# Kernel tuning notes

Measured on AMD Instinct MI355X. Metric: run time of the kernel, lower is better.

## Reference

```python
import jax, jax.numpy as jnp
import numpy as np


def _gru_scan(xg, w_hh, b_hh, h0):
    """Scan a GRU (PyTorch gate order r,z,n) over time. xg: (T,B,3H) precomputed input projections."""
    def step(h, g):
        gh = h @ w_hh.T + b_hh
        i_r, i_z, i_n = jnp.split(g, 3, axis=-1)
        h_r, h_z, h_n = jnp.split(gh, 3, axis=-1)
        r = jax.nn.sigmoid(i_r + h_r)
        z = jax.nn.sigmoid(i_z + h_z)
        n = jnp.tanh(i_n + r * h_n)
        h_new = (1.0 - z) * n + z * h
        return h_new, h_new
    _, ys = jax.lax.scan(step, h0, xg)
    return ys  # (T, B, H)


def setup_inputs() -> dict:
    key = jax.random.key(0)
    ks = jax.random.split(key, 13)
    B, M, T = 64, 80, 2000
    C, H, K = 256, 256, 5
    s = 0.1
    return {
        "x": jax.random.normal(ks[0], (B, M, T), jnp.float32),
        "conv_w": jax.random.normal(ks[1], (C, M, K), jnp.float32) * s,
        "conv_b": jax.random.normal(ks[2], (C,), jnp.float32) * s,
        "w_ih_f": jax.random.normal(ks[3], (3 * H, C), jnp.float32) * s,
        "w_hh_f": jax.random.normal(ks[4], (3 * H, H), jnp.float32) * s,
        "b_ih_f": jax.random.normal(ks[5], (3 * H,), jnp.float32) * s,
        "b_hh_f": jax.random.normal(ks[6], (3 * H,), jnp.float32) * s,
        "w_ih_r": jax.random.normal(ks[7], (3 * H, C), jnp.float32) * s,
        "w_hh_r": jax.random.normal(ks[8], (3 * H, H), jnp.float32) * s,
        "b_ih_r": jax.random.normal(ks[9], (3 * H,), jnp.float32) * s,
        "b_hh_r": jax.random.normal(ks[10], (3 * H,), jnp.float32) * s,
        "clf_w": jax.random.normal(ks[11], (2, 2 * H), jnp.float32) * s,
        "clf_b": jax.random.normal(ks[12], (2,), jnp.float32) * s,
        "window_size": 100,
    }


def reference(x, conv_w, conv_b, w_ih_f, w_hh_f, b_ih_f, b_hh_f,
              w_ih_r, w_hh_r, b_ih_r, b_hh_r, clf_w, clf_b, window_size):
    # Streaming (inference_mode) branch of KWSNet, expressed incrementally:
    # per-step sliding-window conv == full valid conv; the 'bidirectional' GRU
    # with seq_len=1 per step and carried hidden == two independent GRUs both
    # scanned forward in time (one with the _reverse weight set).
    B = x.shape[0]
    K = conv_w.shape[-1]
    H = w_hh_f.shape[-1]
    # Conv1d valid + ReLU: (B, C, Tc), Tc = T - K + 1
    y = jax.lax.conv_general_dilated(x, conv_w, (1,), 'VALID',
                                     dimension_numbers=('NCH', 'OIH', 'NCH'))
    y = jax.nn.relu(y + conv_b[None, :, None])
    seq = jnp.transpose(y, (2, 0, 1))  # (Tc, B, C)
    h0 = jnp.zeros((B, H), seq.dtype)
    xg_f = seq @ w_ih_f.T + b_ih_f  # (Tc, B, 3H)
    xg_r = seq @ w_ih_r.T + b_ih_r
    enc = jnp.concatenate([
        _gru_scan(xg_f, w_hh_f, b_hh_f, h0),
        _gru_scan(xg_r, w_hh_r, b_hh_r, h0),
    ], axis=-1)  # (Tc, B, 2H)
    # Sliding mean over the last W encoder outputs (W = window_size - K + 1)
    W = window_size - K + 1
    cs = jnp.concatenate([jnp.zeros_like(enc[:1]), jnp.cumsum(enc, axis=0)], axis=0)
    means = (cs[W:] - cs[:-W]) / W  # (Tout, B, 2H), Tout = T - window_size + 1
    out = means @ clf_w.T + clf_b  # (Tout, B, 2)
    # torch stacks per-step (1, B, 2) outputs -> (Tout, 1, B, 2)
    return out[:, None, :, :]
```

## Files before the change

kernel.cpp:

```cpp
#include <hip/hip_runtime.h>
#include <hip/hip_bf16.h>


#define TT    2000
#define TC    1996
#define NB    64
#define MCH   80
#define NH    256
#define NN    1536
#define TOUT  1901
#define TCH   250
#define NCHK  8
#define CROWS (TCH * NB)

typedef _Float16 h2_t __attribute__((ext_vector_type(2)));
typedef _Float16 h8_t __attribute__((ext_vector_type(8)));
typedef float    f4_t __attribute__((ext_vector_type(4)));

#define WQSCALE 254.0f
#define INV8    (1.0f / (254.0f * 127.0f))

#define OFF_SEQC ((size_t)0)
#define OFF_XG   ((size_t)8192000)
#define OFF_WT   ((size_t)57344000)
#define OFF_WCAT ((size_t)57753600)
#define OFF_PSUM ((size_t)58540032)
#define OFF_HST  ((size_t)59561984)
#define OFF_WQ   ((size_t)59693056)
#define OFF_ENC  ((size_t)60086272)

__global__ void prep_kernel(const float* __restrict__ conv_w,
                            const float* __restrict__ wihf,
                            const float* __restrict__ wihr,
                            const float* __restrict__ whhf,
                            const float* __restrict__ whhr,
                            float* __restrict__ wT,
                            _Float16* __restrict__ wcat,
                            unsigned* __restrict__ wq) {
    int idx = blockIdx.x * 256 + threadIdx.x;
    if (idx < 400 * 256) {
        int c = idx & 255, mk = idx >> 8;
        wT[idx] = conv_w[c * 400 + mk];
    }
    int i2 = idx - 400 * 256;
    if (i2 >= 0 && i2 < NN * 256) {
        int k = i2 & 255, n = i2 >> 8;
        float v = (n < 768) ? wihf[n * 256 + k] : wihr[(n - 768) * 256 + k];
        wcat[i2] = (_Float16)v;
    }
    int i4 = idx - (400 * 256 + NN * 256);
    if (i4 >= 0 && i4 < 2 * 3 * 256 * 64) {
        int r  = i4 & 255;
        int j  = (i4 >> 8) & 63;
        int dg = i4 >> 14;
        const float* whh = (dg >= 3) ? whhr : whhf;
        int g = (dg >= 3) ? dg - 3 : dg;
        const float* wp = whh + (size_t)(g * 256 + r) * 256 + 4 * j;
        unsigned v = 0;
#pragma unroll
        for (int kk = 0; kk < 4; ++kk) {
            float q = rintf(wp[kk] * WQSCALE);
            q = fminf(fmaxf(q, -127.f), 127.f);
            v |= ((unsigned)((int)q & 0xFF)) << (8 * kk);
        }
        wq[((size_t)dg * 256 + r) * 64 + j] = v;
    }
}

__global__ __launch_bounds__(256, 2)
void conv_kernel(const float* __restrict__ x, const float* __restrict__ wT,
                 const float* __restrict__ conv_b, _Float16* __restrict__ seqc,
                 int t_base, int t_len) {
    __shared__ float xs[MCH][68];
    int tile = blockIdx.x;
    int b    = blockIdx.y;
    int tid  = threadIdx.x;
    for (int idx = tid; idx < MCH * 68; idx += 256) {
        int m = idx / 68, i = idx - m * 68;
        int tt = t_base + tile * 64 + i;
        xs[m][i] = (tt < TT) ? x[(size_t)b * (MCH * TT) + m * TT + tt] : 0.f;
    }
    __syncthreads();
    int lane = tid & 63, tg = tid >> 6;
    float acc[4][16];
#pragma unroll
    for (int cq = 0; cq < 4; ++cq)
#pragma unroll
        for (int t = 0; t < 16; ++t) acc[cq][t] = 0.f;

    for (int m = 0; m < MCH; ++m) {
        float xr_[20];
#pragma unroll
        for (int q = 0; q < 5; ++q) {
            float4 v = *(const float4*)&xs[m][tg * 16 + q * 4];
            xr_[q * 4 + 0] = v.x; xr_[q * 4 + 1] = v.y;
            xr_[q * 4 + 2] = v.z; xr_[q * 4 + 3] = v.w;
        }
#pragma unroll
        for (int cq = 0; cq < 4; ++cq) {
            int c = lane + cq * 64;
            const float* wp = wT + (size_t)(m * 5) * 256 + c;
            float w0_ = wp[0], w1_ = wp[256], w2_ = wp[512], w3_ = wp[768], w4_ = wp[1024];
#pragma unroll
            for (int t = 0; t < 16; ++t)
                acc[cq][t] += w0_ * xr_[t] + w1_ * xr_[t + 1] + w2_ * xr_[t + 2]
                            + w3_ * xr_[t + 3] + w4_ * xr_[t + 4];
        }
    }
#pragma unroll
    for (int cq = 0; cq < 4; ++cq) {
        int c = lane + cq * 64;
        float cb = conv_b[c];
        for (int t = 0; t < 16; ++t) {
            int tl = tile * 64 + tg * 16 + t;
            if (tl < t_len) {
                float v = acc[cq][t] + cb;
                v = v > 0.f ? v : 0.f;
                seqc[((size_t)tl * 64 + b) * 256 + c] = (_Float16)v;
            }
        }
    }
}

__global__ __launch_bounds__(256, 2)
void proj_kernel(const _Float16* __restrict__ seqc, const _Float16* __restrict__ wcat,
                 const float* __restrict__ bihf, const float* __restrict__ bihr,
                 _Float16* __restrict__ xg) {
    __shared__ __align__(16) _Float16 As[128][72];
    __shared__ __align__(16) _Float16 Bs[128][72];
    int row0 = blockIdx.x * 128;
    int n0   = blockIdx.y * 128;
    int tid  = threadIdx.x;
    int lane = tid & 63, wv = tid >> 6;
    int wr = wv >> 1, wc = wv & 1;
    int fm = lane & 15, fq = lane >> 4;
    f4_t acc[4][4];
#pragma unroll
    for (int mt = 0; mt < 4; ++mt)
#pragma unroll
        for (int nt = 0; nt < 4; ++nt) acc[mt][nt] = (f4_t){0.f, 0.f, 0.f, 0.f};

    int r = tid >> 1, part = tid & 1;
    for (int kc = 0; kc < 4; ++kc) {
        const uint4* srcA = (const uint4*)&seqc[(size_t)(row0 + r) * 256 + kc * 64 + part * 32];
        const uint4* srcB = (const uint4*)&wcat[(size_t)(n0 + r) * 256 + kc * 64 + part * 32];
        uint4* dstA = (uint4*)&As[r][part * 32];
        uint4* dstB = (uint4*)&Bs[r][part * 32];
        dstA[0] = srcA[0]; dstA[1] = srcA[1]; dstA[2] = srcA[2]; dstA[3] = srcA[3];
        dstB[0] = srcB[0]; dstB[1] = srcB[1]; dstB[2] = srcB[2]; dstB[3] = srcB[3];
        __syncthreads();
#pragma unroll
        for (int ks = 0; ks < 64; ks += 32) {
            h8_t af[4], bf[4];
#pragma unroll
            for (int mt = 0; mt < 4; ++mt)
                af[mt] = *(const h8_t*)&As[wr * 64 + mt * 16 + fm][ks + fq * 8];
#pragma unroll
            for (int nt = 0; nt < 4; ++nt)
                bf[nt] = *(const h8_t*)&Bs[wc * 64 + nt * 16 + fm][ks + fq * 8];
#pragma unroll
            for (int mt = 0; mt < 4; ++mt)
#pragma unroll
                for (int nt = 0; nt < 4; ++nt)
                    acc[mt][nt] = __builtin_amdgcn_mfma_f32_16x16x32_f16(
                        af[mt], bf[nt], acc[mt][nt], 0, 0, 0);
        }
        __syncthreads();
    }
#pragma unroll
    for (int nt = 0; nt < 4; ++nt) {
        int col = n0 + wc * 64 + nt * 16 + fm;
        int d = (col < 768) ? 0 : 1;
        int j = col - d * 768;
        float bias = d ? bihr[j] : bihf[j];
        size_t obase = (size_t)d * CROWS * 768 + j;
#pragma unroll
        for (int mt = 0; mt < 4; ++mt) {
            int row = row0 + wr * 64 + mt * 16 + fq * 4;
#pragma unroll
            for (int rr = 0; rr < 4; ++rr)
                xg[obase + (size_t)(row + rr) * 768] = (_Float16)(acc[mt][nt][rr] + bias);
        }
    }
}

#define SD4(a, b, c) __builtin_amdgcn_sdot4((int)(a), (int)(b), (c), false)
#define PIN4(v) asm volatile("" : "+v"((v).x), "+v"((v).y), "+v"((v).z), "+v"((v).w))

__global__ __launch_bounds__(256)
void scan_kernel(const _Float16* __restrict__ xg, const uint4* __restrict__ wq,
                 const float* __restrict__ bhhf, const float* __restrict__ bhhr,
                 float* __restrict__ hstate, _Float16* __restrict__ encc,
                 int t0, int len, int first) {
    int blk = blockIdx.x;
    int d = blk >> 6, b = blk & 63;
    int i = threadIdx.x;
    const float* bhh = d ? bhhr : bhhf;

    __shared__ __align__(16) uint4 lwr[16][256];
    __shared__ __align__(16) uint4 lwz[16][256];
    __shared__ __align__(16) unsigned hq8[2][64];

    uint4 wn[16];
    {
        const uint4* pr = wq + ((size_t)(d * 3 + 0) * 256 + i) * 16;
        const uint4* pz = wq + ((size_t)(d * 3 + 1) * 256 + i) * 16;
        const uint4* pn = wq + ((size_t)(d * 3 + 2) * 256 + i) * 16;
#pragma unroll
        for (int k = 0; k < 16; ++k) {
            lwr[k][i] = pr[k];
            lwz[k][i] = pz[k];
            wn[k] = pn[k];
        }
#pragma unroll
        for (int k = 0; k < 16; ++k) PIN4(wn[k]);
    }
    float bhr = bhh[i], bhz = bhh[256 + i], bhn = bhh[512 + i];
    float h = first ? 0.f : hstate[(size_t)blk * 256 + i];

    ((char*)&hq8[0][0])[i] = (char)(int)rintf(h * 127.f);
    __syncthreads();

    const _Float16* xgp = xg + (size_t)d * CROWS * 768 + (size_t)b * 768 + i;
    float xr = (float)xgp[0], xz = (float)xgp[256], xn = (float)xgp[512];
    xgp += (size_t)64 * 768;
    _Float16* ep = encc + (size_t)b * 512 + d * 256 + i;

    int cur = 0;
    for (int t = 0; t < len; ++t) {
        float pxr = (float)xgp[0], pxz = (float)xgp[256], pxn = (float)xgp[512];
        xgp += (size_t)64 * 768;

        const uint4* hqp = (const uint4*)&hq8[cur][0];
        int i0 = 0, i1 = 0, i2 = 0;
#pragma unroll
        for (int k = 0; k < 16; ++k) {
            uint4 hv = hqp[k];
            uint4 wr_ = lwr[k][i];
            uint4 wz_ = lwz[k][i];
            i0 = SD4(wr_.x, hv.x, i0); i0 = SD4(wr_.y, hv.y, i0);
            i0 = SD4(wr_.z, hv.z, i0); i0 = SD4(wr_.w, hv.w, i0);
            i1 = SD4(wz_.x, hv.x, i1); i1 = SD4(wz_.y, hv.y, i1);
            i1 = SD4(wz_.z, hv.z, i1); i1 = SD4(wz_.w, hv.w, i1);
            i2 = SD4(wn[k].x, hv.x, i2); i2 = SD4(wn[k].y, hv.y, i2);
            i2 = SD4(wn[k].z, hv.z, i2); i2 = SD4(wn[k].w, hv.w, i2);
        }

        float hr = (float)i0 * INV8 + bhr;
        float hz = (float)i1 * INV8 + bhz;
        float hn = (float)i2 * INV8 + bhn;
        float rg = 1.f / (1.f + __expf(-(xr + hr)));
        float zg = 1.f / (1.f + __expf(-(xz + hz)));
        float xnr = xn + rg * hn;
        float nv = 1.f - 2.f / (__expf(2.f * xnr) + 1.f);
        h = (1.f - zg) * nv + zg * h;

        int nxt = cur ^ 1;
        ((char*)&hq8[nxt][0])[i] = (char)(int)rintf(h * 127.f);
        ep[(size_t)t * 64 * 512] = (_Float16)h;
        __syncthreads();
        cur = nxt;
        xr = pxr; xz = pxz; xn = pxn;
    }
    hstate[(size_t)blk * 256 + i] = h;
}

__global__ __launch_bounds__(256)
void clf_kernel(const _Float16* __restrict__ encc, const float* __restrict__ clf_w,
                float* __restrict__ psum, int t0, int len) {
    int w = (blockIdx.x * 256 + threadIdx.x) >> 6;
    int lane = threadIdx.x & 63;
    if (w >= len * 64) return;
    const _Float16* row = encc + (size_t)w * 512 + lane * 8;
    uint4 v = *(const uint4*)row;
    float4 c0a = *(const float4*)(clf_w + lane * 8);
    float4 c0b = *(const float4*)(clf_w + lane * 8 + 4);
    float4 c1a = *(const float4*)(clf_w + 512 + lane * 8);
    float4 c1b = *(const float4*)(clf_w + 512 + lane * 8 + 4);
    h2_t e0 = __builtin_bit_cast(h2_t, v.x), e1 = __builtin_bit_cast(h2_t, v.y);
    h2_t e2 = __builtin_bit_cast(h2_t, v.z), e3 = __builtin_bit_cast(h2_t, v.w);
    float s0 = c0a.x * (float)e0[0] + c0a.y * (float)e0[1] + c0a.z * (float)e1[0] + c0a.w * (float)e1[1]
             + c0b.x * (float)e2[0] + c0b.y * (float)e2[1] + c0b.z * (float)e3[0] + c0b.w * (float)e3[1];
    float s1 = c1a.x * (float)e0[0] + c1a.y * (float)e0[1] + c1a.z * (float)e1[0] + c1a.w * (float)e1[1]
             + c1b.x * (float)e2[0] + c1b.y * (float)e2[1] + c1b.z * (float)e3[0] + c1b.w * (float)e3[1];
#pragma unroll
    for (int off = 32; off; off >>= 1) {
        s0 += __shfl_xor(s0, off, 64);
        s1 += __shfl_xor(s1, off, 64);
    }
    if (lane == 0) {
        int tl = w >> 6, b = w & 63;
        psum[((size_t)(t0 + tl) * 64 + b) * 2 + 0] = s0;
        psum[((size_t)(t0 + tl) * 64 + b) * 2 + 1] = s1;
    }
}

__global__ void final_kernel(const float* __restrict__ psum, const float* __restrict__ clf_b,
                             const int* __restrict__ win, float* __restrict__ out) {
    int idx = blockIdx.x * 256 + threadIdx.x;
    if (idx >= TOUT * 128) return;
    int c = idx & 1;
    int rem = idx >> 1;
    int b = rem & 63;
    int tau = rem >> 6;
    int W = win[0] - 5 + 1;
    float s = 0.f;
    for (int j = 0; j < W; ++j)
        s += psum[((size_t)(tau + j) * 64 + b) * 2 + c];
    out[idx] = s / (float)W + clf_b[c];
}

extern "C" void kernel_launch(void* const* d_in, const int* in_sizes, int n_in,
                              void* d_out, int out_size, void* d_ws, size_t ws_size,
                              hipStream_t stream) {
    const float* x      = (const float*)d_in[0];
    const float* conv_w = (const float*)d_in[1];
    const float* conv_b = (const float*)d_in[2];
    const float* w_ih_f = (const float*)d_in[3];
    const float* w_hh_f = (const float*)d_in[4];
    const float* b_ih_f = (const float*)d_in[5];
    const float* b_hh_f = (const float*)d_in[6];
    const float* w_ih_r = (const float*)d_in[7];
    const float* w_hh_r = (const float*)d_in[8];
    const float* b_ih_r = (const float*)d_in[9];
    const float* b_hh_r = (const float*)d_in[10];
    const float* clf_w  = (const float*)d_in[11];
    const float* clf_b  = (const float*)d_in[12];
    const int*   win    = (const int*)d_in[13];
    float* out = (float*)d_out;

    char* ws = (char*)d_ws;
    _Float16* seqc = (_Float16*)(ws + OFF_SEQC);
    _Float16* xg   = (_Float16*)(ws + OFF_XG);
    float*    wT   = (float*)(ws + OFF_WT);
    _Float16* wcat = (_Float16*)(ws + OFF_WCAT);
    float*    psum = (float*)(ws + OFF_PSUM);
    float*    hst  = (float*)(ws + OFF_HST);
    unsigned* wq   = (unsigned*)(ws + OFF_WQ);
    _Float16* encc = (_Float16*)(ws + OFF_ENC);

    int prep_elems = 400 * 256 + NN * 256 + 2 * 3 * 256 * 64;
    prep_kernel<<<(prep_elems + 255) / 256, 256, 0, stream>>>(
        conv_w, w_ih_f, w_ih_r, w_hh_f, w_hh_r, wT, wcat, wq);

    for (int c = 0; c < NCHK; ++c) {
        int t0  = c * TCH;
        int len = (c == NCHK - 1) ? (TC - t0) : TCH;
        conv_kernel<<<dim3(4, 64), 256, 0, stream>>>(x, wT, conv_b, seqc, t0, len);
        proj_kernel<<<dim3(len * 64 / 128, 12), 256, 0, stream>>>(seqc, wcat, b_ih_f, b_ih_r, xg);
        scan_kernel<<<128, 256, 0, stream>>>(xg, (const uint4*)wq, b_hh_f, b_hh_r,
                                             hst, encc, t0, len, c == 0);
        clf_kernel<<<len * 16, 256, 0, stream>>>(encc, clf_w, psum, t0, len);
    }
    final_kernel<<<(TOUT * 128 + 255) / 256, 256, 0, stream>>>(psum, clf_b, win, out);
}
```

Baseline: 2.888 ms.

## Fuse classifier into GRU scan and broadcast hidden state via readlane

The classifier dot product is now computed inside the scan kernel each step, using a wave shuffle reduction plus a cross-wave reduction through shared memory. Per-direction partial sums go to a psum2 buffer that final_kernel adds together, so the encoder fp16 writes and the separate clf_kernel launches go away. The recurrent matvec now reads the quantized hidden state once per lane and broadcasts it with readlane instead of repeated LDS vector loads. The z-gate weights move out of LDS and are reloaded from global or cache every step. This adds serial reduction work to the critical path of every step and raises register pressure from the 32 broadcast values.

```diff
diff --git a/kernel.cpp b/kernel.cpp
--- a/kernel.cpp
+++ b/kernel.cpp
@@ -27,7 +27,7 @@
 #define OFF_PSUM ((size_t)58540032)
 #define OFF_HST  ((size_t)59561984)
 #define OFF_WQ   ((size_t)59693056)
-#define OFF_ENC  ((size_t)60086272)
+#define OFF_PS2  ((size_t)60086272)
 
 __global__ void prep_kernel(const float* __restrict__ conv_w,
                             const float* __restrict__ wihf,
@@ -190,32 +190,31 @@
 __global__ __launch_bounds__(256)
 void scan_kernel(const _Float16* __restrict__ xg, const uint4* __restrict__ wq,
                  const float* __restrict__ bhhf, const float* __restrict__ bhhr,
-                 float* __restrict__ hstate, _Float16* __restrict__ encc,
+                 const float* __restrict__ clfw,
+                 float* __restrict__ hstate, float* __restrict__ psum2,
                  int t0, int len, int first) {
     int blk = blockIdx.x;
     int d = blk >> 6, b = blk & 63;
     int i = threadIdx.x;
+    int lane = i & 63, wv = i >> 6;
     const float* bhh = d ? bhhr : bhhf;
 
     __shared__ __align__(16) uint4 lwr[16][256];
-    __shared__ __align__(16) uint4 lwz[16][256];
     __shared__ __align__(16) unsigned hq8[2][64];
+    __shared__ float cwp[2][4][2];
 
     uint4 wn[16];
+    const uint4* pz = wq + ((size_t)(d * 3 + 1) * 256 + i) * 16;
     {
         const uint4* pr = wq + ((size_t)(d * 3 + 0) * 256 + i) * 16;
-        const uint4* pz = wq + ((size_t)(d * 3 + 1) * 256 + i) * 16;
         const uint4* pn = wq + ((size_t)(d * 3 + 2) * 256 + i) * 16;
 #pragma unroll
-        for (int k = 0; k < 16; ++k) {
-            lwr[k][i] = pr[k];
-            lwz[k][i] = pz[k];
-            wn[k] = pn[k];
-        }
+        for (int k = 0; k < 16; ++k) { lwr[k][i] = pr[k]; wn[k] = pn[k]; }
 #pragma unroll
         for (int k = 0; k < 16; ++k) PIN4(wn[k]);
     }
     float bhr = bhh[i], bhz = bhh[256 + i], bhn = bhh[512 + i];
+    float cw0 = clfw[d * 256 + i], cw1 = clfw[512 + d * 256 + i];
     float h = first ? 0.f : hstate[(size_t)blk * 256 + i];
 
     ((char*)&hq8[0][0])[i] = (char)(int)rintf(h * 127.f);
@@ -224,26 +223,32 @@
     const _Float16* xgp = xg + (size_t)d * CROWS * 768 + (size_t)b * 768 + i;
     float xr = (float)xgp[0], xz = (float)xgp[256], xn = (float)xgp[512];
     xgp += (size_t)64 * 768;
-    _Float16* ep = encc + (size_t)b * 512 + d * 256 + i;
 
     int cur = 0;
     for (int t = 0; t < len; ++t) {
         float pxr = (float)xgp[0], pxz = (float)xgp[256], pxn = (float)xgp[512];
         xgp += (size_t)64 * 768;
 
-        const uint4* hqp = (const uint4*)&hq8[cur][0];
+        unsigned hv = hq8[cur][lane];
         int i0 = 0, i1 = 0, i2 = 0;
-#pragma unroll
-        for (int k = 0; k < 16; ++k) {
-            uint4 hv = hqp[k];
-            uint4 wr_ = lwr[k][i];
-            uint4 wz_ = lwz[k][i];
-            i0 = SD4(wr_.x, hv.x, i0); i0 = SD4(wr_.y, hv.y, i0);
-            i0 = SD4(wr_.z, hv.z, i0); i0 = SD4(wr_.w, hv.w, i0);
-            i1 = SD4(wz_.x, hv.x, i1); i1 = SD4(wz_.y, hv.y, i1);
-            i1 = SD4(wz_.z, hv.z, i1); i1 = SD4(wz_.w, hv.w, i1);
-            i2 = SD4(wn[k].x, hv.x, i2); i2 = SD4(wn[k].y, hv.y, i2);
-            i2 = SD4(wn[k].z, hv.z, i2); i2 = SD4(wn[k].w, hv.w, i2);
+        unsigned hs[32];
+#pragma unroll
+        for (int half = 0; half < 2; ++half) {
+#pragma unroll
+            for (int l = 0; l < 32; ++l)
+                hs[l] = (unsigned)__builtin_amdgcn_readlane((int)hv, half * 32 + l);
+#pragma unroll
+            for (int k = 0; k < 8; ++k) {
+                int kk = half * 8 + k;
+                uint4 wz_ = pz[kk];
+                uint4 wr_ = lwr[kk][i];
+                i0 = SD4(wr_.x, hs[4*k+0], i0); i0 = SD4(wr_.y, hs[4*k+1], i0);
+                i0 = SD4(wr_.z, hs[4*k+2], i0); i0 = SD4(wr_.w, hs[4*k+3], i0);
+                i2 = SD4(wn[kk].x, hs[4*k+0], i2); i2 = SD4(wn[kk].y, hs[4*k+1], i2);
+                i2 = SD4(wn[kk].z, hs[4*k+2], i2); i2 = SD4(wn[kk].w, hs[4*k+3], i2);
+                i1 = SD4(wz_.x, hs[4*k+0], i1); i1 = SD4(wz_.y, hs[4*k+1], i1);
+                i1 = SD4(wz_.z, hs[4*k+2], i1); i1 = SD4(wz_.w, hs[4*k+3], i1);
+            }
         }
 
         float hr = (float)i0 * INV8 + bhr;
@@ -255,47 +260,29 @@
         float nv = 1.f - 2.f / (__expf(2.f * xnr) + 1.f);
         h = (1.f - zg) * nv + zg * h;
 
+        float s0 = cw0 * h, s1 = cw1 * h;
+#pragma unroll
+        for (int off = 32; off; off >>= 1) {
+            s0 += __shfl_xor(s0, off, 64);
+            s1 += __shfl_xor(s1, off, 64);
+        }
         int nxt = cur ^ 1;
         ((char*)&hq8[nxt][0])[i] = (char)(int)rintf(h * 127.f);
-        ep[(size_t)t * 64 * 512] = (_Float16)h;
+        if (lane == 0) { cwp[nxt][wv][0] = s0; cwp[nxt][wv][1] = s1; }
         __syncthreads();
+        if (i == 0) {
+            float a0 = cwp[nxt][0][0] + cwp[nxt][1][0] + cwp[nxt][2][0] + cwp[nxt][3][0];
+            float a1 = cwp[nxt][0][1] + cwp[nxt][1][1] + cwp[nxt][2][1] + cwp[nxt][3][1];
+            float* pp = psum2 + (((size_t)d * TC + (t0 + t)) * 64 + b) * 2;
+            pp[0] = a0; pp[1] = a1;
+        }
         cur = nxt;
         xr = pxr; xz = pxz; xn = pxn;
     }
     hstate[(size_t)blk * 256 + i] = h;
 }
 
-__global__ __launch_bounds__(256)
-void clf_kernel(const _Float16* __restrict__ encc, const float* __restrict__ clf_w,
-                float* __restrict__ psum, int t0, int len) {
-    int w = (blockIdx.x * 256 + threadIdx.x) >> 6;
-    int lane = threadIdx.x & 63;
-    if (w >= len * 64) return;
-    const _Float16* row = encc + (size_t)w * 512 + lane * 8;
-    uint4 v = *(const uint4*)row;
-    float4 c0a = *(const float4*)(clf_w + lane * 8);
-    float4 c0b = *(const float4*)(clf_w + lane * 8 + 4);
-    float4 c1a = *(const float4*)(clf_w + 512 + lane * 8);
-    float4 c1b = *(const float4*)(clf_w + 512 + lane * 8 + 4);
-    h2_t e0 = __builtin_bit_cast(h2_t, v.x), e1 = __builtin_bit_cast(h2_t, v.y);
-    h2_t e2 = __builtin_bit_cast(h2_t, v.z), e3 = __builtin_bit_cast(h2_t, v.w);
-    float s0 = c0a.x * (float)e0[0] + c0a.y * (float)e0[1] + c0a.z * (float)e1[0] + c0a.w * (float)e1[1]
-             + c0b.x * (float)e2[0] + c0b.y * (float)e2[1] + c0b.z * (float)e3[0] + c0b.w * (float)e3[1];
-    float s1 = c1a.x * (float)e0[0] + c1a.y * (float)e0[1] + c1a.z * (float)e1[0] + c1a.w * (float)e1[1]
-             + c1b.x * (float)e2[0] + c1b.y * (float)e2[1] + c1b.z * (float)e3[0] + c1b.w * (float)e3[1];
-#pragma unroll
-    for (int off = 32; off; off >>= 1) {
-        s0 += __shfl_xor(s0, off, 64);
-        s1 += __shfl_xor(s1, off, 64);
-    }
-    if (lane == 0) {
-        int tl = w >> 6, b = w & 63;
-        psum[((size_t)(t0 + tl) * 64 + b) * 2 + 0] = s0;
-        psum[((size_t)(t0 + tl) * 64 + b) * 2 + 1] = s1;
-    }
-}
-
-__global__ void final_kernel(const float* __restrict__ psum, const float* __restrict__ clf_b,
+__global__ void final_kernel(const float* __restrict__ psum2, const float* __restrict__ clf_b,
                              const int* __restrict__ win, float* __restrict__ out) {
     int idx = blockIdx.x * 256 + threadIdx.x;
     if (idx >= TOUT * 128) return;
@@ -304,9 +291,13 @@
     int b = rem & 63;
     int tau = rem >> 6;
     int W = win[0] - 5 + 1;
+    const float* p0 = psum2;
+    const float* p1 = psum2 + (size_t)TC * 64 * 2;
     float s = 0.f;
-    for (int j = 0; j < W; ++j)
-        s += psum[((size_t)(tau + j) * 64 + b) * 2 + c];
+    for (int j = 0; j < W; ++j) {
+        size_t o = ((size_t)(tau + j) * 64 + b) * 2 + c;
+        s += p0[o] + p1[o];
+    }
     out[idx] = s / (float)W + clf_b[c];
 }
 
@@ -334,10 +325,9 @@
     _Float16* xg   = (_Float16*)(ws + OFF_XG);
     float*    wT   = (float*)(ws + OFF_WT);
     _Float16* wcat = (_Float16*)(ws + OFF_WCAT);
-    float*    psum = (float*)(ws + OFF_PSUM);
     float*    hst  = (float*)(ws + OFF_HST);
     unsigned* wq   = (unsigned*)(ws + OFF_WQ);
-    _Float16* encc = (_Float16*)(ws + OFF_ENC);
+    float*    ps2  = (float*)(ws + OFF_PS2);
 
     int prep_elems = 400 * 256 + NN * 256 + 2 * 3 * 256 * 64;
     prep_kernel<<<(prep_elems + 255) / 256, 256, 0, stream>>>(
@@ -348,9 +338,8 @@
         int len = (c == NCHK - 1) ? (TC - t0) : TCH;
         conv_kernel<<<dim3(4, 64), 256, 0, stream>>>(x, wT, conv_b, seqc, t0, len);
         proj_kernel<<<dim3(len * 64 / 128, 12), 256, 0, stream>>>(seqc, wcat, b_ih_f, b_ih_r, xg);
-        scan_kernel<<<128, 256, 0, stream>>>(xg, (const uint4*)wq, b_hh_f, b_hh_r,
-                                             hst, encc, t0, len, c == 0);
-        clf_kernel<<<len * 16, 256, 0, stream>>>(encc, clf_w, psum, t0, len);
-    }
-    final_kernel<<<(TOUT * 128 + 255) / 256, 256, 0, stream>>>(psum, clf_b, win, out);
-}
+        scan_kernel<<<128, 256, 0, stream>>>(xg, (const uint4*)wq, b_hh_f, b_hh_r, clf_w,
+                                             hst, ps2, t0, len, c == 0);
+    }
+    final_kernel<<<(TOUT * 128 + 255) / 256, 256, 0, stream>>>(ps2, clf_b, win, out);
+}
```

Measured after the change: 3.197 ms. 10.7% more time.
